# Optimization experiments

Measured on AMD Instinct MI355X. Metric: run time of the kernel, lower is better.

## Reference

```python
import jax, jax.numpy as jnp
import numpy as np

N_EMBD = 1024
HEAD_SIZE = 64

def setup_inputs() -> dict:
    key = jax.random.key(0)
    k1, k2, k3, k4 = jax.random.split(key, 4)
    x = jax.random.normal(k1, (8, 2048, N_EMBD), dtype=jnp.float32)
    s = 1.0 / np.sqrt(N_EMBD)
    Wk = jax.random.normal(k2, (HEAD_SIZE, N_EMBD), dtype=jnp.float32) * s
    Wq = jax.random.normal(k3, (HEAD_SIZE, N_EMBD), dtype=jnp.float32) * s
    Wv = jax.random.normal(k4, (HEAD_SIZE, N_EMBD), dtype=jnp.float32) * s
    return {"x": x, "Wk": Wk, "Wq": Wq, "Wv": Wv}

def reference(x, Wk, Wq, Wv):
    B, T, C = x.shape
    k = jnp.einsum('btc,hc->bth', x, Wk)  # [B,T,Hd]
    q = jnp.einsum('btc,hc->bth', x, Wq)
    v = jnp.einsum('btc,hc->bth', x, Wv)
    # NOTE: original scales by C**-0.5 where C = n_embd (not head_size)
    wei = jnp.einsum('bqh,bkh->bqk', q, k) * (C ** -0.5)  # [B,T,T]
    causal = jnp.tril(jnp.ones((T, T), dtype=bool))
    wei = jnp.where(causal, wei, -jnp.inf)
    wei = jax.nn.softmax(wei, axis=-1)
    out = jnp.einsum('bqk,bkh->bqh', wei, v)  # [B,T,Hd]
    return out
```

## Files before the change

kernel.cpp:

```cpp
#include <hip/hip_runtime.h>


typedef __attribute__((ext_vector_type(4))) short sv4;
typedef __attribute__((ext_vector_type(8))) short sv8;
typedef __attribute__((ext_vector_type(4))) float f32x4;

#define NB   8
#define TSEQ 2048
#define CDIM 1024
#define HD   64
#define MROWS (NB * TSEQ)

__device__ __forceinline__ short f2s(float f) {
  union { float f; unsigned u; } v; v.f = f;
  unsigned u = v.u;
  u += 0x7fffu + ((u >> 16) & 1u);
  return (short)(u >> 16);
}
__device__ __forceinline__ unsigned pk2(float lo, float hi) {
  return (unsigned)(unsigned short)f2s(lo) | ((unsigned)(unsigned short)f2s(hi) << 16);
}
__device__ __forceinline__ void glds16(const short* g, short* l) {
  __builtin_amdgcn_global_load_lds(
      (const __attribute__((address_space(1))) unsigned int*)g,
      (__attribute__((address_space(3))) unsigned int*)l, 16, 0, 0);
}

__global__ __launch_bounds__(256) void wcvt(
    const float* __restrict__ Wq, const float* __restrict__ Wk,
    const float* __restrict__ Wv, short* __restrict__ wb)
{
  int i = blockIdx.x * 256 + threadIdx.x;
  int t = i / 3072;
  int rem = i - t * 3072;
  int r = rem >> 4, s = rem & 15;
  int j = r >> 6, wrow = r & 63;
  const float* W = (j == 0) ? Wq : (j == 1) ? Wk : Wv;
  const float* src = W + (size_t)wrow * CDIM + t * 128 + ((s ^ (wrow & 7)) << 3);
  float4 a = *(const float4*)src;
  float4 b = *(const float4*)(src + 4);
  sv8 v = {f2s(a.x), f2s(a.y), f2s(a.z), f2s(a.w),
           f2s(b.x), f2s(b.y), f2s(b.z), f2s(b.w)};
  *(sv8*)(wb + (size_t)i * 8) = v;
}

__global__ __launch_bounds__(1024) void qkv_proj(
    const float* __restrict__ x,
    const short* __restrict__ wb,
    short* __restrict__ qw,
    short* __restrict__ kw,
    short* __restrict__ vtw)
{
  __shared__ short wlds[2][24576];
  __shared__ short xlds[2][8192];
  const int tid  = threadIdx.x;
  const int wid  = tid >> 6;
  const int lane = tid & 63;
  const int g    = lane >> 4;
  const int c16  = lane & 15;
  const int rowg = wid >> 2;
  const int ph   = wid & 3;
  const int row0 = blockIdx.x * 64;

  const int xr = tid >> 4, xs = tid & 15;
  const float* xsrc = x + (size_t)(row0 + xr) * CDIM + xs * 8;
  const int xwo = xr * 128 + ((xs ^ (xr & 7)) << 3);

  const int arow = rowg * 16 + c16;
  const int x7   = arow & 7;
  int rWo[3], rW7[3];
  #pragma unroll
  for (int p6 = 0; p6 < 3; ++p6) {
    int p = ph * 3 + p6;
    int r = (p >> 2) * 64 + (p & 3) * 16 + c16;
    rWo[p6] = r * 128;
    rW7[p6] = r & 7;
  }

  f32x4 acc[3];
  #pragma unroll
  for (int p6 = 0; p6 < 3; ++p6) acc[p6] = (f32x4){0.f, 0.f, 0.f, 0.f};

  float4 px[2][2];

  #pragma unroll
  for (int k2 = 0; k2 < 3; ++k2)
    glds16(wb + (size_t)(tid + k2 * 1024) * 8, &wlds[0][(tid + k2 * 1024) * 8]);
  px[0][0] = *(const float4*)(xsrc);
  px[0][1] = *(const float4*)(xsrc + 4);
  px[1][0] = *(const float4*)(xsrc + 128);
  px[1][1] = *(const float4*)(xsrc + 132);
  asm volatile("s_waitcnt vmcnt(2)" ::: "memory");
  {
    float4 A = px[0][0], B = px[0][1];
    sv8 v = {f2s(A.x), f2s(A.y), f2s(A.z), f2s(A.w),
             f2s(B.x), f2s(B.y), f2s(B.z), f2s(B.w)};
    *(sv8*)&xlds[0][xwo] = v;
  }
  asm volatile("s_waitcnt lgkmcnt(0)" ::: "memory");
  __builtin_amdgcn_sched_barrier(0);
  __builtin_amdgcn_s_barrier();

  #pragma unroll
  for (int t = 0; t < 8; ++t) {
    const int buf = t & 1;
    if (t < 7) {
      #pragma unroll
      for (int k2 = 0; k2 < 3; ++k2)
        glds16(wb + (size_t)((t + 1) * 3072 + tid + k2 * 1024) * 8,
               &wlds[buf ^ 1][(tid + k2 * 1024) * 8]);
    }
    if (t < 6) {
      px[t & 1][0] = *(const float4*)(xsrc + (t + 2) * 128);
      px[t & 1][1] = *(const float4*)(xsrc + (t + 2) * 128 + 4);
    }
    if (t < 7) {
      float4 A = px[(t + 1) & 1][0], B = px[(t + 1) & 1][1];
      sv8 v = {f2s(A.x), f2s(A.y), f2s(A.z), f2s(A.w),
               f2s(B.x), f2s(B.y), f2s(B.z), f2s(B.w)};
      *(sv8*)&xlds[buf ^ 1][xwo] = v;
    }
    #pragma unroll
    for (int kk = 0; kk < 4; ++kk) {
      int kslot = kk * 4 + g;
      sv8 a = *(const sv8*)&xlds[buf][arow * 128 + ((kslot ^ x7) << 3)];
      #pragma unroll
      for (int p6 = 0; p6 < 3; ++p6) {
        sv8 bfr = *(const sv8*)&wlds[buf][rWo[p6] + ((kslot ^ rW7[p6]) << 3)];
        acc[p6] = __builtin_amdgcn_mfma_f32_16x16x32_bf16(a, bfr, acc[p6], 0, 0, 0);
      }
    }
    if (t < 7) {
      if (t < 6) asm volatile("s_waitcnt vmcnt(2) lgkmcnt(0)" ::: "memory");
      else       asm volatile("s_waitcnt vmcnt(0) lgkmcnt(0)" ::: "memory");
      __builtin_amdgcn_sched_barrier(0);
      __builtin_amdgcn_s_barrier();
    }
  }

  #pragma unroll
  for (int p6 = 0; p6 < 3; ++p6) {
    int p = ph * 3 + p6, j = p >> 2, n = p & 3;
    int cc  = (n << 4) + c16;
    int rr0 = row0 + rowg * 16 + (g << 2);
    if (j == 2) {
      int b = rr0 >> 11, ti = rr0 & (TSEQ - 1);
      int kt = ti >> 6, key = ti & 63;
      sv4 v = {f2s(acc[p6][0]), f2s(acc[p6][1]), f2s(acc[p6][2]), f2s(acc[p6][3])};
      *(sv4*)&vtw[(((size_t)b * 32 + kt) * 64 + cc) * 64 +
                  ((((key >> 3) ^ (cc & 7)) << 3) | (key & 7))] = v;
    } else {
      #pragma unroll
      for (int r = 0; r < 4; ++r) {
        int rr = rr0 + r;
        if (j == 0) {
          qw[(size_t)rr * HD + cc] = f2s(acc[p6][r] * 0.03125f);
        } else {
          kw[(size_t)rr * HD + ((((cc >> 3) ^ (rr & 7)) << 3) | (cc & 7))] =
              f2s(acc[p6][r]);
        }
      }
    }
  }
}

__global__ __launch_bounds__(512) void attn(
    const short* __restrict__ qw,
    const short* __restrict__ kw,
    const short* __restrict__ vtw,
    float* __restrict__ out)
{
  __shared__ short kbuf[2][2][8192];
  __shared__ short vbuf[2][2][8192];
  __shared__ short bridge[8][1024];

  const int tid  = threadIdx.x;
  const int wid  = tid >> 6;
  const int h    = wid >> 2;
  const int lwid = wid & 3;
  const int ltid = tid & 255;
  const int lane = tid & 63;
  const int g    = lane >> 4;
  const int c16  = lane & 15;

  const int bid   = blockIdx.x;
  const int batch = bid & 7;
  const int qb    = bid >> 3;
  const int q0    = qb << 6;
  const size_t base = (size_t)batch * TSEQ * HD;

  const int ntot = (qb >> 1) + 1;
  const int th_  = (ntot + 1) >> 1;
  const int t0   = h ? th_ : 0;
  const int cnt  = h ? (ntot - th_) : th_;

  const int qrow = q0 + (lwid << 4) + c16;
  sv8 qa0 = *(const sv8*)(qw + base + (size_t)qrow * HD + (g << 3));
  sv8 qa1 = *(const sv8*)(qw + base + (size_t)qrow * HD + 32 + (g << 3));

  float m = -1e30f, l = 0.f;
  f32x4 o[4];
  #pragma unroll
  for (int n = 0; n < 4; ++n) o[n] = (f32x4){0.f, 0.f, 0.f, 0.f};

  short* br = &bridge[wid][0];
  const int sx7 = c16 & 7;

  #define STAGE(tt, bb)                                                        \
    {                                                                          \
      const short* ksrc = kw + base + (size_t)(tt) * 8192;                     \
      const short* vsrc = vtw + ((size_t)batch * 32 + (tt) * 2) * 4096;        \
      _Pragma("unroll")                                                        \
      for (int q = 0; q < 4; ++q)                                              \
        glds16(ksrc + (ltid + q * 256) * 8, &kbuf[h][bb][(ltid + q * 256) * 8]);\
      _Pragma("unroll")                                                        \
      for (int q = 0; q < 4; ++q)                                              \
        glds16(vsrc + (ltid + q * 256) * 8, &vbuf[h][bb][(ltid + q * 256) * 8]);\
    }

  if (cnt > 0) STAGE(t0, 0);
  asm volatile("s_waitcnt vmcnt(0)" ::: "memory");
  __builtin_amdgcn_s_barrier();

  for (int it = 0; it < th_; ++it) {
    const int t   = t0 + it;
    const int buf = it & 1;
    const bool valid = it < cnt;
    if (valid && (it + 1 < cnt)) STAGE(t + 1, buf ^ 1);

    if (valid) {
      f32x4 s[8];
      #pragma unroll
      for (int n = 0; n < 8; ++n) s[n] = (f32x4){0.f, 0.f, 0.f, 0.f};
      __builtin_amdgcn_s_setprio(1);
      #pragma unroll
      for (int n = 0; n < 8; ++n) {
        int kr = (n << 4) + c16;
        sv8 k0 = *(const sv8*)&kbuf[h][buf][kr * 64 + ((g ^ (kr & 7)) << 3)];
        s[n] = __builtin_amdgcn_mfma_f32_16x16x32_bf16(k0, qa0, s[n], 0, 0, 0);
        sv8 k1 = *(const sv8*)&kbuf[h][buf][kr * 64 + (((4 + g) ^ (kr & 7)) << 3)];
        s[n] = __builtin_amdgcn_mfma_f32_16x16x32_bf16(k1, qa1, s[n], 0, 0, 0);
      }
      __builtin_amdgcn_s_setprio(0);

      if (t == (qb >> 1)) {
        #pragma unroll
        for (int n = 0; n < 8; ++n) {
          int key = (t << 7) + (n << 4) + (g << 2);
          #pragma unroll
          for (int r = 0; r < 4; ++r)
            s[n][r] = (key + r <= qrow) ? s[n][r] : -1e30f;
        }
      }

      float pmax = -1e30f;
      #pragma unroll
      for (int n = 0; n < 8; ++n)
        pmax = fmaxf(pmax, fmaxf(fmaxf(s[n][0], s[n][1]), fmaxf(s[n][2], s[n][3])));
      float mnew  = m;
      const bool defer = (__all(pmax - m <= 8.0f) != 0);
      if (!defer) {
        float mx = fmaxf(pmax, __shfl_xor(pmax, 16));
        mx = fmaxf(mx, __shfl_xor(mx, 32));
        mnew = fmaxf(m, mx);
      }

      float sum = 0.f;
      #pragma unroll
      for (int n = 0; n < 8; ++n) {
        #pragma unroll
        for (int r = 0; r < 4; ++r) {
          float p = __expf(s[n][r] - mnew);
          s[n][r] = p;
          sum += p;
        }
      }
      sum += __shfl_xor(sum, 16);
      sum += __shfl_xor(sum, 32);

      if (!defer) {
        float alpha = __expf(m - mnew);
        m = mnew;
        l = l * alpha + sum;
        float af[4];
        #pragma unroll
        for (int r = 0; r < 4; ++r) af[r] = __shfl(alpha, (g << 2) + r);
        #pragma unroll
        for (int n = 0; n < 4; ++n)
          #pragma unroll
          for (int r = 0; r < 4; ++r) o[n][r] *= af[r];
      } else {
        l += sum;
      }

      #pragma unroll
      for (int hv = 0; hv < 2; ++hv) {
        #pragma unroll
        for (int n = 0; n < 4; ++n) {
          int nn = (hv << 2) + n;
          int slot = 2 * n + (g >> 1);
          uint2 w2;
          w2.x = pk2(s[nn][0], s[nn][1]);
          w2.y = pk2(s[nn][2], s[nn][3]);
          *(uint2*)&br[(c16 << 6) + ((slot ^ sx7) << 3) + ((g & 1) << 2)] = w2;
        }
        asm volatile("s_waitcnt lgkmcnt(0)" ::: "memory");
        __builtin_amdgcn_sched_barrier(0);
        __builtin_amdgcn_s_setprio(1);
        #pragma unroll
        for (int kk = 0; kk < 2; ++kk) {
          int kslot = (((hv << 1) + kk) << 2) + g;
          sv8 pa = *(const sv8*)&br[(c16 << 6) + ((((kk << 2) + g) ^ sx7) << 3)];
          #pragma unroll
          for (int n = 0; n < 4; ++n) {
            int vr = (n << 4) + c16;
            sv8 vf = *(const sv8*)&vbuf[h][buf][(kslot >> 3) * 4096 + vr * 64 +
                                               (((kslot & 7) ^ (vr & 7)) << 3)];
            o[n] = __builtin_amdgcn_mfma_f32_16x16x32_bf16(pa, vf, o[n], 0, 0, 0);
          }
        }
        __builtin_amdgcn_s_setprio(0);
      }
    }

    asm volatile("s_waitcnt vmcnt(0)" ::: "memory");
    __builtin_amdgcn_sched_barrier(0);
    __builtin_amdgcn_s_barrier();
  }

  float* OLDS = (float*)&kbuf[0][0][0];
  float* mlds = OLDS + 4096;
  float* llds = mlds + 64;

  if (h == 1) {
    #pragma unroll
    for (int n = 0; n < 4; ++n) {
      #pragma unroll
      for (int r = 0; r < 4; ++r) {
        int row = (lwid << 4) + (g << 2) + r;
        OLDS[row * 64 + (n << 4) + c16] = o[n][r];
      }
    }
    if (lane < 16) {
      mlds[(lwid << 4) + lane] = m;
      llds[(lwid << 4) + lane] = l;
    }
  }
  __syncthreads();
  if (h == 0) {
    #pragma unroll
    for (int r = 0; r < 4; ++r) {
      int row = (lwid << 4) + (g << 2) + r;
      float m0 = __shfl(m, (g << 2) + r);
      float l0 = __shfl(l, (g << 2) + r);
      float m1 = mlds[row], l1 = llds[row];
      float M  = fmaxf(m0, m1);
      float a0 = __expf(m0 - M), a1 = __expf(m1 - M);
      float invL = 1.f / (l0 * a0 + l1 * a1);
      #pragma unroll
      for (int n = 0; n < 4; ++n) {
        float v = (o[n][r] * a0 + OLDS[row * 64 + (n << 4) + c16] * a1) * invL;
        out[base + (size_t)(q0 + row) * HD + (n << 4) + c16] = v;
      }
    }
  }
  #undef STAGE
}

extern "C" void kernel_launch(void* const* d_in, const int* in_sizes, int n_in,
                              void* d_out, int out_size, void* d_ws, size_t ws_size,
                              hipStream_t stream) {
  const float* x  = (const float*)d_in[0];
  const float* Wk = (const float*)d_in[1];
  const float* Wq = (const float*)d_in[2];
  const float* Wv = (const float*)d_in[3];
  float* out = (float*)d_out;

  short* qw  = (short*)d_ws;
  short* kw  = qw + (size_t)MROWS * HD;
  short* vtw = kw + (size_t)MROWS * HD;
  short* wb  = vtw + (size_t)NB * HD * TSEQ;

  wcvt<<<dim3(96), dim3(256), 0, stream>>>(Wq, Wk, Wv, wb);
  qkv_proj<<<dim3(MROWS / 64), dim3(1024), 0, stream>>>(x, wb, qw, kw, vtw);
  attn<<<dim3(256), dim3(512), 0, stream>>>(qw, kw, vtw, out);
}
```

Before: 49.19 us.

## Halve QKV projection block size and K-tile, reuse weight fragments across two row tiles

Measured after the change: 52.59 us. 1.07x slower.

```diff
diff --git a/kernel.cpp b/kernel.cpp
--- a/kernel.cpp
+++ b/kernel.cpp
@@ -31,12 +31,12 @@
     const float* __restrict__ Wv, short* __restrict__ wb)
 {
   int i = blockIdx.x * 256 + threadIdx.x;
-  int t = i / 3072;
-  int rem = i - t * 3072;
-  int r = rem >> 4, s = rem & 15;
+  int t = i / 1536;
+  int rem = i - t * 1536;
+  int r = rem >> 3, s = rem & 7;
   int j = r >> 6, wrow = r & 63;
   const float* W = (j == 0) ? Wq : (j == 1) ? Wk : Wv;
-  const float* src = W + (size_t)wrow * CDIM + t * 128 + ((s ^ (wrow & 7)) << 3);
+  const float* src = W + (size_t)wrow * CDIM + t * 64 + ((s ^ (wrow & 7)) << 3);
   float4 a = *(const float4*)src;
   float4 b = *(const float4*)(src + 4);
   sv8 v = {f2s(a.x), f2s(a.y), f2s(a.z), f2s(a.w),
@@ -44,52 +44,56 @@
   *(sv8*)(wb + (size_t)i * 8) = v;
 }
 
-__global__ __launch_bounds__(1024) void qkv_proj(
+__global__ __launch_bounds__(512) void qkv_proj(
     const float* __restrict__ x,
     const short* __restrict__ wb,
     short* __restrict__ qw,
     short* __restrict__ kw,
     short* __restrict__ vtw)
 {
-  __shared__ short wlds[2][24576];
-  __shared__ short xlds[2][8192];
+  __shared__ short wlds[2][12288];
+  __shared__ short xlds[2][4096];
   const int tid  = threadIdx.x;
   const int wid  = tid >> 6;
   const int lane = tid & 63;
   const int g    = lane >> 4;
   const int c16  = lane & 15;
-  const int rowg = wid >> 2;
-  const int ph   = wid & 3;
+  const int rowg = wid & 1;
+  const int ph   = wid >> 1;
   const int row0 = blockIdx.x * 64;
 
-  const int xr = tid >> 4, xs = tid & 15;
+  const int xr = tid >> 3, xs = tid & 7;
   const float* xsrc = x + (size_t)(row0 + xr) * CDIM + xs * 8;
-  const int xwo = xr * 128 + ((xs ^ (xr & 7)) << 3);
-
-  const int arow = rowg * 16 + c16;
-  const int x7   = arow & 7;
+  const int xwo = xr * 64 + ((xs ^ (xr & 7)) << 3);
+
+  const int arow0 = rowg * 16 + c16;
+  const int arow1 = 32 + rowg * 16 + c16;
+  const int a0x = arow0 & 7, a1x = arow1 & 7;
   int rWo[3], rW7[3];
   #pragma unroll
   for (int p6 = 0; p6 < 3; ++p6) {
     int p = ph * 3 + p6;
     int r = (p >> 2) * 64 + (p & 3) * 16 + c16;
-    rWo[p6] = r * 128;
+    rWo[p6] = r * 64;
     rW7[p6] = r & 7;
   }
 
-  f32x4 acc[3];
-  #pragma unroll
-  for (int p6 = 0; p6 < 3; ++p6) acc[p6] = (f32x4){0.f, 0.f, 0.f, 0.f};
+  f32x4 acc[2][3];
+  #pragma unroll
+  for (int rf = 0; rf < 2; ++rf)
+    #pragma unroll
+    for (int p6 = 0; p6 < 3; ++p6)
+      acc[rf][p6] = (f32x4){0.f, 0.f, 0.f, 0.f};
 
   float4 px[2][2];
 
   #pragma unroll
   for (int k2 = 0; k2 < 3; ++k2)
-    glds16(wb + (size_t)(tid + k2 * 1024) * 8, &wlds[0][(tid + k2 * 1024) * 8]);
+    glds16(wb + (size_t)(tid + k2 * 512) * 8, &wlds[0][(tid + k2 * 512) * 8]);
   px[0][0] = *(const float4*)(xsrc);
   px[0][1] = *(const float4*)(xsrc + 4);
-  px[1][0] = *(const float4*)(xsrc + 128);
-  px[1][1] = *(const float4*)(xsrc + 132);
+  px[1][0] = *(const float4*)(xsrc + 64);
+  px[1][1] = *(const float4*)(xsrc + 68);
   asm volatile("s_waitcnt vmcnt(2)" ::: "memory");
   {
     float4 A = px[0][0], B = px[0][1];
@@ -102,62 +106,68 @@
   __builtin_amdgcn_s_barrier();
 
   #pragma unroll
-  for (int t = 0; t < 8; ++t) {
+  for (int t = 0; t < 16; ++t) {
     const int buf = t & 1;
-    if (t < 7) {
+    if (t < 15) {
       #pragma unroll
       for (int k2 = 0; k2 < 3; ++k2)
-        glds16(wb + (size_t)((t + 1) * 3072 + tid + k2 * 1024) * 8,
-               &wlds[buf ^ 1][(tid + k2 * 1024) * 8]);
-    }
-    if (t < 6) {
-      px[t & 1][0] = *(const float4*)(xsrc + (t + 2) * 128);
-      px[t & 1][1] = *(const float4*)(xsrc + (t + 2) * 128 + 4);
-    }
-    if (t < 7) {
+        glds16(wb + (size_t)((t + 1) * 1536 + tid + k2 * 512) * 8,
+               &wlds[buf ^ 1][(tid + k2 * 512) * 8]);
+    }
+    if (t < 14) {
+      px[t & 1][0] = *(const float4*)(xsrc + (t + 2) * 64);
+      px[t & 1][1] = *(const float4*)(xsrc + (t + 2) * 64 + 4);
+    }
+    if (t < 15) {
       float4 A = px[(t + 1) & 1][0], B = px[(t + 1) & 1][1];
       sv8 v = {f2s(A.x), f2s(A.y), f2s(A.z), f2s(A.w),
                f2s(B.x), f2s(B.y), f2s(B.z), f2s(B.w)};
       *(sv8*)&xlds[buf ^ 1][xwo] = v;
     }
     #pragma unroll
-    for (int kk = 0; kk < 4; ++kk) {
-      int kslot = kk * 4 + g;
-      sv8 a = *(const sv8*)&xlds[buf][arow * 128 + ((kslot ^ x7) << 3)];
+    for (int kk = 0; kk < 2; ++kk) {
+      int slot = kk * 4 + g;
+      sv8 a0 = *(const sv8*)&xlds[buf][arow0 * 64 + ((slot ^ a0x) << 3)];
+      sv8 a1 = *(const sv8*)&xlds[buf][arow1 * 64 + ((slot ^ a1x) << 3)];
       #pragma unroll
       for (int p6 = 0; p6 < 3; ++p6) {
-        sv8 bfr = *(const sv8*)&wlds[buf][rWo[p6] + ((kslot ^ rW7[p6]) << 3)];
-        acc[p6] = __builtin_amdgcn_mfma_f32_16x16x32_bf16(a, bfr, acc[p6], 0, 0, 0);
-      }
-    }
-    if (t < 7) {
-      if (t < 6) asm volatile("s_waitcnt vmcnt(2) lgkmcnt(0)" ::: "memory");
-      else       asm volatile("s_waitcnt vmcnt(0) lgkmcnt(0)" ::: "memory");
+        sv8 bfr = *(const sv8*)&wlds[buf][rWo[p6] + ((slot ^ rW7[p6]) << 3)];
+        acc[0][p6] = __builtin_amdgcn_mfma_f32_16x16x32_bf16(a0, bfr, acc[0][p6], 0, 0, 0);
+        acc[1][p6] = __builtin_amdgcn_mfma_f32_16x16x32_bf16(a1, bfr, acc[1][p6], 0, 0, 0);
+      }
+    }
+    if (t < 15) {
+      if (t < 14) asm volatile("s_waitcnt vmcnt(2) lgkmcnt(0)" ::: "memory");
+      else        asm volatile("s_waitcnt vmcnt(0) lgkmcnt(0)" ::: "memory");
       __builtin_amdgcn_sched_barrier(0);
       __builtin_amdgcn_s_barrier();
     }
   }
 
   #pragma unroll
-  for (int p6 = 0; p6 < 3; ++p6) {
-    int p = ph * 3 + p6, j = p >> 2, n = p & 3;
-    int cc  = (n << 4) + c16;
-    int rr0 = row0 + rowg * 16 + (g << 2);
-    if (j == 2) {
-      int b = rr0 >> 11, ti = rr0 & (TSEQ - 1);
-      int kt = ti >> 6, key = ti & 63;
-      sv4 v = {f2s(acc[p6][0]), f2s(acc[p6][1]), f2s(acc[p6][2]), f2s(acc[p6][3])};
-      *(sv4*)&vtw[(((size_t)b * 32 + kt) * 64 + cc) * 64 +
-                  ((((key >> 3) ^ (cc & 7)) << 3) | (key & 7))] = v;
-    } else {
-      #pragma unroll
-      for (int r = 0; r < 4; ++r) {
-        int rr = rr0 + r;
-        if (j == 0) {
-          qw[(size_t)rr * HD + cc] = f2s(acc[p6][r] * 0.03125f);
-        } else {
-          kw[(size_t)rr * HD + ((((cc >> 3) ^ (rr & 7)) << 3) | (cc & 7))] =
-              f2s(acc[p6][r]);
+  for (int rf = 0; rf < 2; ++rf) {
+    #pragma unroll
+    for (int p6 = 0; p6 < 3; ++p6) {
+      int p = ph * 3 + p6, j = p >> 2, n = p & 3;
+      int cc  = (n << 4) + c16;
+      int rr0 = row0 + rf * 32 + rowg * 16 + (g << 2);
+      if (j == 2) {
+        int b = rr0 >> 11, ti = rr0 & (TSEQ - 1);
+        int kt = ti >> 6, key = ti & 63;
+        sv4 v = {f2s(acc[rf][p6][0]), f2s(acc[rf][p6][1]),
+                 f2s(acc[rf][p6][2]), f2s(acc[rf][p6][3])};
+        *(sv4*)&vtw[(((size_t)b * 32 + kt) * 64 + cc) * 64 +
+                    ((((key >> 3) ^ (cc & 7)) << 3) | (key & 7))] = v;
+      } else {
+        #pragma unroll
+        for (int r = 0; r < 4; ++r) {
+          int rr = rr0 + r;
+          if (j == 0) {
+            qw[(size_t)rr * HD + cc] = f2s(acc[rf][p6][r] * 0.03125f);
+          } else {
+            kw[(size_t)rr * HD + ((((cc >> 3) ^ (rr & 7)) << 3) | (cc & 7))] =
+                f2s(acc[rf][p6][r]);
+          }
         }
       }
     }
@@ -382,6 +392,6 @@
   short* wb  = vtw + (size_t)NB * HD * TSEQ;
 
   wcvt<<<dim3(96), dim3(256), 0, stream>>>(Wq, Wk, Wv, wb);
-  qkv_proj<<<dim3(MROWS / 64), dim3(1024), 0, stream>>>(x, wb, qw, kw, vtw);
+  qkv_proj<<<dim3(MROWS / 64), dim3(512), 0, stream>>>(x, wb, qw, kw, vtw);
   attn<<<dim3(256), dim3(512), 0, stream>>>(qw, kw, vtw, out);
 }
```

## Double QKV projection row tile to 128 rows per block to reuse weight tiles

Applied to the files above, without the earlier changes.

Result: slower. 53.73 us (+9.2%).

```diff
diff --git a/kernel.cpp b/kernel.cpp
--- a/kernel.cpp
+++ b/kernel.cpp
@@ -52,22 +52,25 @@
     short* __restrict__ vtw)
 {
   __shared__ short wlds[2][24576];
-  __shared__ short xlds[2][8192];
+  __shared__ short xlds[2][16384];
   const int tid  = threadIdx.x;
   const int wid  = tid >> 6;
   const int lane = tid & 63;
   const int g    = lane >> 4;
   const int c16  = lane & 15;
-  const int rowg = wid >> 2;
-  const int ph   = wid & 3;
-  const int row0 = blockIdx.x * 64;
-
-  const int xr = tid >> 4, xs = tid & 15;
-  const float* xsrc = x + (size_t)(row0 + xr) * CDIM + xs * 8;
-  const int xwo = xr * 128 + ((xs ^ (xr & 7)) << 3);
-
-  const int arow = rowg * 16 + c16;
-  const int x7   = arow & 7;
+  const int rowg = wid & 3;
+  const int ph   = wid >> 2;
+  const int row0 = blockIdx.x * 128;
+
+  const int xr = tid >> 3, xs = tid & 7;
+  const float* xsrc = x + (size_t)(row0 + xr) * CDIM + xs * 16;
+  const int xk   = xr & 7;
+  const int xwo0 = xr * 128 + (((2 * xs)     ^ xk) << 3);
+  const int xwo1 = xr * 128 + (((2 * xs + 1) ^ xk) << 3);
+
+  const int arow0 = rowg * 32 + c16;
+  const int arow1 = arow0 + 16;
+  const int ax = arow0 & 7;
   int rWo[3], rW7[3];
   #pragma unroll
   for (int p6 = 0; p6 < 3; ++p6) {
@@ -77,26 +80,35 @@
     rW7[p6] = r & 7;
   }
 
-  f32x4 acc[3];
-  #pragma unroll
-  for (int p6 = 0; p6 < 3; ++p6) acc[p6] = (f32x4){0.f, 0.f, 0.f, 0.f};
-
-  float4 px[2][2];
+  f32x4 acc[2][3];
+  #pragma unroll
+  for (int rf = 0; rf < 2; ++rf)
+    #pragma unroll
+    for (int p6 = 0; p6 < 3; ++p6)
+      acc[rf][p6] = (f32x4){0.f, 0.f, 0.f, 0.f};
+
+  float4 px[2][4];
+
+  #define XWRITE(bb, pb)                                                     \
+    {                                                                        \
+      float4 A = px[pb][0], B = px[pb][1], C = px[pb][2], D = px[pb][3];     \
+      sv8 v0 = {f2s(A.x), f2s(A.y), f2s(A.z), f2s(A.w),                     \
+                f2s(B.x), f2s(B.y), f2s(B.z), f2s(B.w)};                    \
+      sv8 v1 = {f2s(C.x), f2s(C.y), f2s(C.z), f2s(C.w),                     \
+                f2s(D.x), f2s(D.y), f2s(D.z), f2s(D.w)};                    \
+      *(sv8*)&xlds[bb][xwo0] = v0;                                           \
+      *(sv8*)&xlds[bb][xwo1] = v1;                                           \
+    }
 
   #pragma unroll
   for (int k2 = 0; k2 < 3; ++k2)
     glds16(wb + (size_t)(tid + k2 * 1024) * 8, &wlds[0][(tid + k2 * 1024) * 8]);
-  px[0][0] = *(const float4*)(xsrc);
-  px[0][1] = *(const float4*)(xsrc + 4);
-  px[1][0] = *(const float4*)(xsrc + 128);
-  px[1][1] = *(const float4*)(xsrc + 132);
-  asm volatile("s_waitcnt vmcnt(2)" ::: "memory");
-  {
-    float4 A = px[0][0], B = px[0][1];
-    sv8 v = {f2s(A.x), f2s(A.y), f2s(A.z), f2s(A.w),
-             f2s(B.x), f2s(B.y), f2s(B.z), f2s(B.w)};
-    *(sv8*)&xlds[0][xwo] = v;
-  }
+  #pragma unroll
+  for (int q = 0; q < 4; ++q) px[0][q] = *(const float4*)(xsrc + q * 4);
+  #pragma unroll
+  for (int q = 0; q < 4; ++q) px[1][q] = *(const float4*)(xsrc + 128 + q * 4);
+  asm volatile("s_waitcnt vmcnt(4)" ::: "memory");
+  XWRITE(0, 0);
   asm volatile("s_waitcnt lgkmcnt(0)" ::: "memory");
   __builtin_amdgcn_sched_barrier(0);
   __builtin_amdgcn_s_barrier();
@@ -111,27 +123,27 @@
                &wlds[buf ^ 1][(tid + k2 * 1024) * 8]);
     }
     if (t < 6) {
-      px[t & 1][0] = *(const float4*)(xsrc + (t + 2) * 128);
-      px[t & 1][1] = *(const float4*)(xsrc + (t + 2) * 128 + 4);
+      #pragma unroll
+      for (int q = 0; q < 4; ++q)
+        px[t & 1][q] = *(const float4*)(xsrc + (t + 2) * 128 + q * 4);
     }
     if (t < 7) {
-      float4 A = px[(t + 1) & 1][0], B = px[(t + 1) & 1][1];
-      sv8 v = {f2s(A.x), f2s(A.y), f2s(A.z), f2s(A.w),
-               f2s(B.x), f2s(B.y), f2s(B.z), f2s(B.w)};
-      *(sv8*)&xlds[buf ^ 1][xwo] = v;
+      XWRITE(buf ^ 1, (t + 1) & 1);
     }
     #pragma unroll
     for (int kk = 0; kk < 4; ++kk) {
-      int kslot = kk * 4 + g;
-      sv8 a = *(const sv8*)&xlds[buf][arow * 128 + ((kslot ^ x7) << 3)];
+      int slot = kk * 4 + g;
+      sv8 a0 = *(const sv8*)&xlds[buf][arow0 * 128 + ((slot ^ ax) << 3)];
+      sv8 a1 = *(const sv8*)&xlds[buf][arow1 * 128 + ((slot ^ ax) << 3)];
       #pragma unroll
       for (int p6 = 0; p6 < 3; ++p6) {
-        sv8 bfr = *(const sv8*)&wlds[buf][rWo[p6] + ((kslot ^ rW7[p6]) << 3)];
-        acc[p6] = __builtin_amdgcn_mfma_f32_16x16x32_bf16(a, bfr, acc[p6], 0, 0, 0);
+        sv8 bfr = *(const sv8*)&wlds[buf][rWo[p6] + ((slot ^ rW7[p6]) << 3)];
+        acc[0][p6] = __builtin_amdgcn_mfma_f32_16x16x32_bf16(a0, bfr, acc[0][p6], 0, 0, 0);
+        acc[1][p6] = __builtin_amdgcn_mfma_f32_16x16x32_bf16(a1, bfr, acc[1][p6], 0, 0, 0);
       }
     }
     if (t < 7) {
-      if (t < 6) asm volatile("s_waitcnt vmcnt(2) lgkmcnt(0)" ::: "memory");
+      if (t < 6) asm volatile("s_waitcnt vmcnt(4) lgkmcnt(0)" ::: "memory");
       else       asm volatile("s_waitcnt vmcnt(0) lgkmcnt(0)" ::: "memory");
       __builtin_amdgcn_sched_barrier(0);
       __builtin_amdgcn_s_barrier();
@@ -139,29 +151,34 @@
   }
 
   #pragma unroll
-  for (int p6 = 0; p6 < 3; ++p6) {
-    int p = ph * 3 + p6, j = p >> 2, n = p & 3;
-    int cc  = (n << 4) + c16;
-    int rr0 = row0 + rowg * 16 + (g << 2);
-    if (j == 2) {
-      int b = rr0 >> 11, ti = rr0 & (TSEQ - 1);
-      int kt = ti >> 6, key = ti & 63;
-      sv4 v = {f2s(acc[p6][0]), f2s(acc[p6][1]), f2s(acc[p6][2]), f2s(acc[p6][3])};
-      *(sv4*)&vtw[(((size_t)b * 32 + kt) * 64 + cc) * 64 +
-                  ((((key >> 3) ^ (cc & 7)) << 3) | (key & 7))] = v;
-    } else {
-      #pragma unroll
-      for (int r = 0; r < 4; ++r) {
-        int rr = rr0 + r;
-        if (j == 0) {
-          qw[(size_t)rr * HD + cc] = f2s(acc[p6][r] * 0.03125f);
-        } else {
-          kw[(size_t)rr * HD + ((((cc >> 3) ^ (rr & 7)) << 3) | (cc & 7))] =
-              f2s(acc[p6][r]);
+  for (int rf = 0; rf < 2; ++rf) {
+    #pragma unroll
+    for (int p6 = 0; p6 < 3; ++p6) {
+      int p = ph * 3 + p6, j = p >> 2, n = p & 3;
+      int cc  = (n << 4) + c16;
+      int rr0 = row0 + rowg * 32 + rf * 16 + (g << 2);
+      if (j == 2) {
+        int b = rr0 >> 11, ti = rr0 & (TSEQ - 1);
+        int kt = ti >> 6, key = ti & 63;
+        sv4 v = {f2s(acc[rf][p6][0]), f2s(acc[rf][p6][1]),
+                 f2s(acc[rf][p6][2]), f2s(acc[rf][p6][3])};
+        *(sv4*)&vtw[(((size_t)b * 32 + kt) * 64 + cc) * 64 +
+                    ((((key >> 3) ^ (cc & 7)) << 3) | (key & 7))] = v;
+      } else {
+        #pragma unroll
+        for (int r = 0; r < 4; ++r) {
+          int rr = rr0 + r;
+          if (j == 0) {
+            qw[(size_t)rr * HD + cc] = f2s(acc[rf][p6][r] * 0.03125f);
+          } else {
+            kw[(size_t)rr * HD + ((((cc >> 3) ^ (rr & 7)) << 3) | (cc & 7))] =
+                f2s(acc[rf][p6][r]);
+          }
         }
       }
     }
   }
+  #undef XWRITE
 }
 
 __global__ __launch_bounds__(512) void attn(
@@ -382,6 +399,6 @@
   short* wb  = vtw + (size_t)NB * HD * TSEQ;
 
   wcvt<<<dim3(96), dim3(256), 0, stream>>>(Wq, Wk, Wv, wb);
-  qkv_proj<<<dim3(MROWS / 64), dim3(1024), 0, stream>>>(x, wb, qw, kw, vtw);
+  qkv_proj<<<dim3(MROWS / 128), dim3(1024), 0, stream>>>(x, wb, qw, kw, vtw);
   attn<<<dim3(256), dim3(512), 0, stream>>>(qw, kw, vtw, out);
 }
```
